# Kernel tuning notes

Measured on AMD Instinct MI355X. Metric: run time of the kernel, lower is better.

The kernel has to match this reference:

```python
import jax, jax.numpy as jnp
import numpy as np
import math

FEAT_DIM = 256
QUERY_DIM = 256
HIDDEN = 64
OUT_DIM = 256
HEADS = 8


def setup_inputs() -> dict:
    key = jax.random.key(0)
    ks = jax.random.split(key, 10)
    B, NQ, NKV = 2, 2048, 2048
    s_q = 1.0 / math.sqrt(QUERY_DIM)
    s_f = 1.0 / math.sqrt(FEAT_DIM)
    s_o = 1.0 / math.sqrt(HIDDEN * HEADS)
    return {
        "feat": jax.random.normal(ks[0], (B, NKV, FEAT_DIM), jnp.float32),
        "query": jax.random.normal(ks[1], (B, NQ, QUERY_DIM), jnp.float32),
        # stacked per-head weights (each head has its own Linear in torch)
        "Wq": jax.random.uniform(ks[2], (HEADS, QUERY_DIM, HIDDEN), jnp.float32, -s_q, s_q),
        "bq": jax.random.uniform(ks[3], (HEADS, HIDDEN), jnp.float32, -s_q, s_q),
        "Wk": jax.random.uniform(ks[4], (HEADS, FEAT_DIM, HIDDEN), jnp.float32, -s_f, s_f),
        "bk": jax.random.uniform(ks[5], (HEADS, HIDDEN), jnp.float32, -s_f, s_f),
        "Wv": jax.random.uniform(ks[6], (HEADS, FEAT_DIM, HIDDEN), jnp.float32, -s_f, s_f),
        "bv": jax.random.uniform(ks[7], (HEADS, HIDDEN), jnp.float32, -s_f, s_f),
        "Wo": jax.random.uniform(ks[8], (HEADS * HIDDEN, OUT_DIM), jnp.float32, -s_o, s_o),
        "bo": jax.random.uniform(ks[9], (OUT_DIM,), jnp.float32, -s_o, s_o),
    }


def reference(feat, query, Wq, bq, Wk, bk, Wv, bv, Wo, bo):
    # Per-head projections, vectorized over the head axis h.
    # q: [B, H, Nq, E]; k, v: [B, H, Nkv, E]
    q = jnp.einsum("bnd,hde->bhne", query, Wq) + bq[None, :, None, :]
    k = jnp.einsum("bnd,hde->bhne", feat, Wk) + bk[None, :, None, :]
    v = jnp.einsum("bnd,hde->bhne", feat, Wv) + bv[None, :, None, :]
    scale = 1.0 / math.sqrt(HIDDEN)
    scores = jnp.einsum("bhqe,bhke->bhqk", q, k) * scale  # [B, H, Nq, Nkv]
    prob = jax.nn.softmax(scores, axis=-1)
    # dropout p=0.0 (eval) -> identity
    heads = jnp.einsum("bhqk,bhke->bhqe", prob, v)  # [B, H, Nq, E]
    # concat heads in order (head 0 first) then output projection
    B, H, NQ, E = heads.shape
    cat = heads.transpose(0, 2, 1, 3).reshape(B, NQ, H * E)
    return cat @ Wo + bo
```

## Files before the change

kernel.cpp:

```cpp
#include <hip/hip_runtime.h>
#include <hip/hip_bf16.h>

typedef unsigned short u16;
typedef __attribute__((ext_vector_type(8))) short short8;
typedef __attribute__((ext_vector_type(4))) float f32x4;
typedef __attribute__((ext_vector_type(16))) float f32x16;
typedef __attribute__((ext_vector_type(2))) int v2i;

#define HEADS 8
#define HID 64
#define QSCALE 0.18033688011112042f

__device__ inline u16 f2bf(float f){
    unsigned u = __float_as_uint(f);
    unsigned r = (u + 0x7fffu + ((u >> 16) & 1u)) >> 16;
    return (u16)r;
}

__device__ inline int cvtpk(float lo, float hi){
    int r;
    asm("v_cvt_pk_bf16_f32 %0, %1, %2" : "=v"(r) : "v"(lo), "v"(hi));
    return r;
}

__device__ inline float exp2fast(float x){
    float r;
    asm("v_exp_f32 %0, %1" : "=v"(r) : "v"(x));
    return r;
}

__device__ inline float xhalf_max(float x){
    v2i r = __builtin_amdgcn_permlane32_swap(__float_as_int(x), __float_as_int(x), false, false);
    return fmaxf(__int_as_float(r.x), __int_as_float(r.y));
}
__device__ inline float xhalf_sum(float x){
    v2i r = __builtin_amdgcn_permlane32_swap(__float_as_int(x), __float_as_int(x), false, false);
    return __int_as_float(r.x) + __int_as_float(r.y);
}

__global__ __launch_bounds__(256) void prep_weights(
    const float* __restrict__ Wq, const float* __restrict__ Wk,
    const float* __restrict__ Wv, const float* __restrict__ Wo,
    u16* __restrict__ WqT, u16* __restrict__ WkT, u16* __restrict__ WvT,
    u16* __restrict__ WoT)
{
    int id = blockIdx.x * 256 + threadIdx.x;
    if (id < 393216) {
        int w = id / 131072;
        int r = id % 131072;
        int c = r >> 8;
        int d = r & 255;
        const float* W = (w == 0) ? Wq : (w == 1 ? Wk : Wv);
        u16* WT = (w == 0) ? WqT : (w == 1 ? WkT : WvT);
        WT[c * 256 + d] = f2bf(W[(c >> 6) * (256 * 64) + d * 64 + (c & 63)]);
    } else {
        int r = id - 393216;
        int o = r >> 9;
        int k = r & 511;
        WoT[o * 512 + k] = f2bf(Wo[k * 256 + o]);
    }
}

__global__ __launch_bounds__(256) void proj_kernel(
    const float* __restrict__ feat, const float* __restrict__ query,
    const u16* __restrict__ WqT, const u16* __restrict__ WkT, const u16* __restrict__ WvT,
    const float* __restrict__ bq, const float* __restrict__ bk, const float* __restrict__ bv,
    u16* __restrict__ Qb, u16* __restrict__ KVf)
{
    int which = blockIdx.z;
    const float* X = (which == 0) ? query : feat;
    const u16* WT = (which == 0) ? WqT : (which == 1 ? WkT : WvT);
    const float* bias = (which == 0) ? bq : (which == 1 ? bk : bv);
    int m0 = blockIdx.x * 64;
    int n0 = blockIdx.y * 64;
    int t = threadIdx.x;
    int lane = t & 63, w = t >> 6;
    int l15 = lane & 15, kof = (lane >> 4) * 8;

    __shared__ __align__(16) u16 lA[64][72];
    __shared__ __align__(16) u16 lB[64][72];

    f32x4 acc[4] = {};
    for (int kt = 0; kt < 256; kt += 64) {
        #pragma unroll
        for (int i = 0; i < 4; i++) {
            int lin = t + i * 256;
            int row = lin >> 4, c4 = (lin & 15) * 4;
            float4 v = *reinterpret_cast<const float4*>(&X[(m0 + row) * 256 + kt + c4]);
            lA[row][c4 + 0] = f2bf(v.x);
            lA[row][c4 + 1] = f2bf(v.y);
            lA[row][c4 + 2] = f2bf(v.z);
            lA[row][c4 + 3] = f2bf(v.w);
        }
        #pragma unroll
        for (int i = 0; i < 2; i++) {
            int lin = t + i * 256;
            int row = lin >> 3, c8 = (lin & 7) * 8;
            *reinterpret_cast<uint4*>(&lB[row][c8]) =
                *reinterpret_cast<const uint4*>(&WT[(n0 + row) * 256 + kt + c8]);
        }
        __syncthreads();
        #pragma unroll
        for (int ks = 0; ks < 2; ks++) {
            short8 a = *reinterpret_cast<const short8*>(&lA[w * 16 + l15][ks * 32 + kof]);
            #pragma unroll
            for (int nt = 0; nt < 4; nt++) {
                short8 b = *reinterpret_cast<const short8*>(&lB[nt * 16 + l15][ks * 32 + kof]);
                acc[nt] = __builtin_amdgcn_mfma_f32_16x16x32_bf16(a, b, acc[nt], 0, 0, 0);
            }
        }
        __syncthreads();
    }
    #pragma unroll
    for (int nt = 0; nt < 4; nt++) {
        #pragma unroll
        for (int i = 0; i < 4; i++) {
            int mrow = m0 + w * 16 + (lane >> 4) * 4 + i;
            int col = n0 + nt * 16 + l15;
            float val = acc[nt][i] + bias[col];
            int b_ = mrow >> 11, n = mrow & 2047;
            int h = col >> 6, e = col & 63;
            int bh = b_ * 8 + h;
            if (which == 0) {
                Qb[(bh * 2048 + n) * 64 + e] = f2bf(val * QSCALE);
            } else {
                int tile = n >> 6, nl = n & 63;
                size_t base = ((size_t)(bh * 32 + tile)) * 8192;
                size_t idx;
                if (which == 1) {
                    int reg  = ((nl >> 5) << 2) | (e >> 4);
                    int ln   = (nl & 31) | (((e >> 3) & 1) << 5);
                    idx = base + reg * 512 + ln * 8 + (e & 7);
                } else {
                    int reg  = ((e >> 5) << 2) | (nl >> 4);
                    int ln   = (e & 31) | (((nl >> 3) & 1) << 5);
                    idx = base + 4096 + reg * 512 + ln * 8 + (nl & 7);
                }
                KVf[idx] = f2bf(val);
            }
        }
    }
}

__global__ __launch_bounds__(512, 2) void attn_kernel(
    const u16* __restrict__ Qb, const u16* __restrict__ KVf, u16* __restrict__ cat)
{
    int lb = blockIdx.x;
    int chunk = lb >> 4;
    int bh = ((lb & 7) << 1) | ((lb >> 3) & 1);
    int b_ = bh >> 3, head = bh & 7;
    int t = threadIdx.x, lane = t & 63, w = t >> 6;
    int l31 = lane & 31, hh = lane >> 5;
    int sp = w >> 1, kvh = w & 1, wi = w >> 1;
    int q0 = chunk * 128 + sp * 32;

    __shared__ __align__(16) u16 smem[34816];
    u16* tiles = smem;
    float* Ol = (float*)smem;
    float* Ml = (float*)(smem + 33792);
    float* Ll = (float*)(smem + 34304);

    const u16* KVfB = KVf + ((size_t)(bh * 32 + kvh * 16)) * 8192;

    short8 qf[4];
    {
        const u16* qp = Qb + (bh * 2048 + q0 + l31) * 64 + hh * 8;
        #pragma unroll
        for (int kc = 0; kc < 4; kc++)
            qf[kc] = *reinterpret_cast<const short8*>(qp + kc * 16);
    }

    f32x16 o0 = {}, o1 = {};
    float mrun = -1e30f, lrun = 0.0f;

#define PACKP(sb, base, out) {                                              \
        int A0 = cvtpk(sb[base+0], sb[base+1]);                             \
        int B0 = cvtpk(sb[base+4], sb[base+5]);                             \
        v2i r0 = __builtin_amdgcn_permlane32_swap(A0, B0, false, false);    \
        int A1 = cvtpk(sb[base+2], sb[base+3]);                             \
        int B1 = cvtpk(sb[base+6], sb[base+7]);                             \
        v2i r1 = __builtin_amdgcn_permlane32_swap(A1, B1, false, false);    \
        union { int i[4]; short8 s; } uu;                                   \
        uu.i[0] = r0.x; uu.i[1] = r1.x; uu.i[2] = r0.y; uu.i[3] = r1.y;     \
        out = uu.s; }

    auto stage = [&](int buf, int tile) {
        const u16* gsrc = KVfB + (size_t)tile * 8192;
        u16* ldst = tiles + (kvh * 2 + buf) * 8192;
        #pragma unroll
        for (int c = 0; c < 4; c++) {
            int off = (wi * 4 + c) * 512 + lane * 8;
            __builtin_amdgcn_global_load_lds(
                (const __attribute__((address_space(1))) unsigned int*)(const void*)(gsrc + off),
                (__attribute__((address_space(3))) unsigned int*)(void*)(ldst + off),
                16, 0, 0);
        }
    };

    stage(0, 0);
    asm volatile("s_waitcnt vmcnt(0)" ::: "memory");
    __syncthreads();

    int cur = 0;
    for (int tt = 0; tt < 16; tt++) {
        if (tt < 15) stage(cur ^ 1, tt + 1);

        const u16* kbase = tiles + (kvh * 2 + cur) * 8192;
        short8 kf[8], vf[8];
        #pragma unroll
        for (int r = 0; r < 8; r++)
            kf[r] = *reinterpret_cast<const short8*>(kbase + r * 512 + lane * 8);
        #pragma unroll
        for (int r = 0; r < 8; r++)
            vf[r] = *reinterpret_cast<const short8*>(kbase + 4096 + r * 512 + lane * 8);

        f32x16 s0 = {}, s1 = {};
        #pragma unroll
        for (int kc = 0; kc < 4; kc++)
            s0 = __builtin_amdgcn_mfma_f32_32x32x16_bf16(kf[kc], qf[kc], s0, 0, 0, 0);
        #pragma unroll
        for (int kc = 0; kc < 4; kc++)
            s1 = __builtin_amdgcn_mfma_f32_32x32x16_bf16(kf[4 + kc], qf[kc], s1, 0, 0, 0);

        float pm[8];
        #pragma unroll
        for (int r = 0; r < 8; r++)
            pm[r] = fmaxf(fmaxf(s0[r], s0[r + 8]), fmaxf(s1[r], s1[r + 8]));
        #pragma unroll
        for (int st = 4; st > 0; st >>= 1)
            #pragma unroll
            for (int r = 0; r < 8; r++) if (r < st) pm[r] = fmaxf(pm[r], pm[r + st]);
        float pmax = xhalf_max(pm[0]);
        if (__any(pmax > mrun + 6.0f)) {
            float mnew = fmaxf(mrun, pmax);
            float corr = exp2fast(mrun - mnew);
            mrun = mnew;
            lrun *= corr;
            #pragma unroll
            for (int r = 0; r < 16; r++) { o0[r] *= corr; o1[r] *= corr; }
        }
        float ac[4] = {0.f, 0.f, 0.f, 0.f};
        #pragma unroll
        for (int r = 0; r < 16; r++) {
            float p0 = exp2fast(s0[r] - mrun);
            float p1 = exp2fast(s1[r] - mrun);
            s0[r] = p0; s1[r] = p1;
            ac[r & 3] += p0 + p1;
        }
        float lsum = (ac[0] + ac[1]) + (ac[2] + ac[3]);
        lrun += xhalf_sum(lsum);

        short8 pf[4];
        PACKP(s0, 0, pf[0]); PACKP(s0, 8, pf[1]);
        PACKP(s1, 0, pf[2]); PACKP(s1, 8, pf[3]);

        #pragma unroll
        for (int c = 0; c < 4; c++) {
            o0 = __builtin_amdgcn_mfma_f32_32x32x16_bf16(vf[c],     pf[c], o0, 0, 0, 0);
            o1 = __builtin_amdgcn_mfma_f32_32x32x16_bf16(vf[4 + c], pf[c], o1, 0, 0, 0);
        }

        asm volatile("s_waitcnt vmcnt(0)" ::: "memory");
        __syncthreads();
        cur ^= 1;
    }

    #pragma unroll
    for (int eb = 0; eb < 2; eb++) {
        #pragma unroll
        for (int r = 0; r < 16; r++) {
            int d = eb * 32 + (r & 3) + 8 * (r >> 2) + 4 * hh;
            Ol[(w * 64 + d) * 33 + l31] = eb ? o1[r] : o0[r];
        }
    }
    if (hh == 0) { Ml[w * 32 + l31] = mrun; Ll[w * 32 + l31] = lrun; }
    __syncthreads();

    {
        int msp = t >> 7;
        int tt2 = t & 127;
        int q = tt2 >> 2;
        int d0 = (tt2 & 3) * 16;
        int wA = msp * 2, wB = msp * 2 + 1;
        float mA = Ml[wA * 32 + q], mB = Ml[wB * 32 + q];
        float ms = fmaxf(mA, mB);
        float scA = exp2fast(mA - ms), scB = exp2fast(mB - ms);
        float lsum = Ll[wA * 32 + q] * scA + Ll[wB * 32 + q] * scB;
        float linv = 1.0f / lsum;
        float vv[16];
        #pragma unroll
        for (int j = 0; j < 16; j++)
            vv[j] = (Ol[(wA * 64 + d0 + j) * 33 + q] * scA +
                     Ol[(wB * 64 + d0 + j) * 33 + q] * scB) * linv;
        uint4 st0, st1;
        st0.x = (unsigned)cvtpk(vv[0],  vv[1]);
        st0.y = (unsigned)cvtpk(vv[2],  vv[3]);
        st0.z = (unsigned)cvtpk(vv[4],  vv[5]);
        st0.w = (unsigned)cvtpk(vv[6],  vv[7]);
        st1.x = (unsigned)cvtpk(vv[8],  vv[9]);
        st1.y = (unsigned)cvtpk(vv[10], vv[11]);
        st1.z = (unsigned)cvtpk(vv[12], vv[13]);
        st1.w = (unsigned)cvtpk(vv[14], vv[15]);
        u16* crow = cat + (b_ * 2048 + chunk * 128 + msp * 32 + q) * 512 + head * 64 + d0;
        *reinterpret_cast<uint4*>(crow) = st0;
        *reinterpret_cast<uint4*>(crow + 8) = st1;
    }
#undef PACKP
}

__global__ __launch_bounds__(256) void outproj_kernel(
    const u16* __restrict__ cat, const u16* __restrict__ WoT,
    const float* __restrict__ bo, float* __restrict__ out)
{
    int m0 = blockIdx.x * 64, n0 = blockIdx.y * 64;
    int t = threadIdx.x, lane = t & 63, w = t >> 6;
    int l15 = lane & 15, kof = (lane >> 4) * 8;

    __shared__ __align__(16) u16 lA[64][72];
    __shared__ __align__(16) u16 lB[64][72];

    f32x4 acc[4] = {};
    for (int kt = 0; kt < 512; kt += 64) {
        #pragma unroll
        for (int i = 0; i < 2; i++) {
            int lin = t + i * 256;
            int row = lin >> 3, c8 = (lin & 7) * 8;
            *reinterpret_cast<uint4*>(&lA[row][c8]) =
                *reinterpret_cast<const uint4*>(&cat[(m0 + row) * 512 + kt + c8]);
            *reinterpret_cast<uint4*>(&lB[row][c8]) =
                *reinterpret_cast<const uint4*>(&WoT[(n0 + row) * 512 + kt + c8]);
        }
        __syncthreads();
        #pragma unroll
        for (int ks = 0; ks < 2; ks++) {
            short8 a = *reinterpret_cast<const short8*>(&lA[w * 16 + l15][ks * 32 + kof]);
            #pragma unroll
            for (int nt = 0; nt < 4; nt++) {
                short8 b = *reinterpret_cast<const short8*>(&lB[nt * 16 + l15][ks * 32 + kof]);
                acc[nt] = __builtin_amdgcn_mfma_f32_16x16x32_bf16(a, b, acc[nt], 0, 0, 0);
            }
        }
        __syncthreads();
    }
    #pragma unroll
    for (int i = 0; i < 4; i++) {
        int mrow = m0 + w * 16 + (lane >> 4) * 4 + i;
        #pragma unroll
        for (int nt = 0; nt < 4; nt++) {
            int col = n0 + nt * 16 + l15;
            out[mrow * 256 + col] = acc[nt][i] + bo[col];
        }
    }
}

extern "C" void kernel_launch(void* const* d_in, const int* in_sizes, int n_in,
                              void* d_out, int out_size, void* d_ws, size_t ws_size,
                              hipStream_t stream) {
    const float* feat  = (const float*)d_in[0];
    const float* query = (const float*)d_in[1];
    const float* Wq = (const float*)d_in[2];
    const float* bq = (const float*)d_in[3];
    const float* Wk = (const float*)d_in[4];
    const float* bk = (const float*)d_in[5];
    const float* Wv = (const float*)d_in[6];
    const float* bv = (const float*)d_in[7];
    const float* Wo = (const float*)d_in[8];
    const float* bo = (const float*)d_in[9];
    float* out = (float*)d_out;

    char* ws = (char*)d_ws;
    u16* WqT = (u16*)(ws + 0);
    u16* WkT = (u16*)(ws + 262144);
    u16* WvT = (u16*)(ws + 524288);
    u16* WoT = (u16*)(ws + 786432);
    u16* Qb  = (u16*)(ws + 1048576);
    u16* KVf = (u16*)(ws + 1048576 + 4194304);
    u16* cat = (u16*)(ws + 1048576 + 12582912);

    hipLaunchKernelGGL(prep_weights, dim3(2048), dim3(256), 0, stream,
                       Wq, Wk, Wv, Wo, WqT, WkT, WvT, WoT);
    hipLaunchKernelGGL(proj_kernel, dim3(64, 8, 3), dim3(256), 0, stream,
                       feat, query, WqT, WkT, WvT, bq, bk, bv, Qb, KVf);
    hipLaunchKernelGGL(attn_kernel, dim3(256), dim3(512), 0, stream,
                       Qb, KVf, cat);
    hipLaunchKernelGGL(outproj_kernel, dim3(64, 4), dim3(256), 0, stream,
                       cat, WoT, bo, out);
}
```

Baseline: 57.62 us.

## Pre-convert activations to bf16 and split attention into smaller 256-thread blocks

Activation fp32->bf16 conversion moves into the prep kernel, so the projection GEMM loads bf16 tiles directly instead of converting them 8-12 times across blocks. The attention kernel is halved to 4 waves and 64 queries per block, doubling the grid to 512 blocks for better CU coverage, at the cost of reloading K/V tiles more often. MFMA sections are also wrapped with s_setprio to favour matrix issue. This adds an extra global round trip for the bf16 activations.

```diff
diff --git a/kernel.cpp b/kernel.cpp
--- a/kernel.cpp
+++ b/kernel.cpp
@@ -39,22 +39,37 @@
 }
 
 __global__ __launch_bounds__(256) void prep_weights(
+    const float* __restrict__ query, const float* __restrict__ feat,
     const float* __restrict__ Wq, const float* __restrict__ Wk,
     const float* __restrict__ Wv, const float* __restrict__ Wo,
+    u16* __restrict__ Xbq, u16* __restrict__ Xbf,
     u16* __restrict__ WqT, u16* __restrict__ WkT, u16* __restrict__ WvT,
     u16* __restrict__ WoT)
 {
     int id = blockIdx.x * 256 + threadIdx.x;
-    if (id < 393216) {
-        int w = id / 131072;
-        int r = id % 131072;
+    if (id < 262144) {
+        const float* src = (id < 131072) ? query : feat;
+        u16* dst = (id < 131072) ? Xbq : Xbf;
+        int r = (id < 131072) ? id : id - 131072;
+        float4 a = *reinterpret_cast<const float4*>(&src[r * 8]);
+        float4 b = *reinterpret_cast<const float4*>(&src[r * 8 + 4]);
+        uint4 s;
+        s.x = (unsigned)cvtpk(a.x, a.y);
+        s.y = (unsigned)cvtpk(a.z, a.w);
+        s.z = (unsigned)cvtpk(b.x, b.y);
+        s.w = (unsigned)cvtpk(b.z, b.w);
+        *reinterpret_cast<uint4*>(&dst[r * 8]) = s;
+    } else if (id < 655360) {
+        int id2 = id - 262144;
+        int w = id2 / 131072;
+        int r = id2 % 131072;
         int c = r >> 8;
         int d = r & 255;
         const float* W = (w == 0) ? Wq : (w == 1 ? Wk : Wv);
         u16* WT = (w == 0) ? WqT : (w == 1 ? WkT : WvT);
         WT[c * 256 + d] = f2bf(W[(c >> 6) * (256 * 64) + d * 64 + (c & 63)]);
     } else {
-        int r = id - 393216;
+        int r = id - 655360;
         int o = r >> 9;
         int k = r & 511;
         WoT[o * 512 + k] = f2bf(Wo[k * 256 + o]);
@@ -62,13 +77,13 @@
 }
 
 __global__ __launch_bounds__(256) void proj_kernel(
-    const float* __restrict__ feat, const float* __restrict__ query,
+    const u16* __restrict__ Xbq, const u16* __restrict__ Xbf,
     const u16* __restrict__ WqT, const u16* __restrict__ WkT, const u16* __restrict__ WvT,
     const float* __restrict__ bq, const float* __restrict__ bk, const float* __restrict__ bv,
     u16* __restrict__ Qb, u16* __restrict__ KVf)
 {
     int which = blockIdx.z;
-    const float* X = (which == 0) ? query : feat;
+    const u16* Xb = (which == 0) ? Xbq : Xbf;
     const u16* WT = (which == 0) ? WqT : (which == 1 ? WkT : WvT);
     const float* bias = (which == 0) ? bq : (which == 1 ? bk : bv);
     int m0 = blockIdx.x * 64;
@@ -83,19 +98,11 @@
     f32x4 acc[4] = {};
     for (int kt = 0; kt < 256; kt += 64) {
         #pragma unroll
-        for (int i = 0; i < 4; i++) {
-            int lin = t + i * 256;
-            int row = lin >> 4, c4 = (lin & 15) * 4;
-            float4 v = *reinterpret_cast<const float4*>(&X[(m0 + row) * 256 + kt + c4]);
-            lA[row][c4 + 0] = f2bf(v.x);
-            lA[row][c4 + 1] = f2bf(v.y);
-            lA[row][c4 + 2] = f2bf(v.z);
-            lA[row][c4 + 3] = f2bf(v.w);
-        }
-        #pragma unroll
         for (int i = 0; i < 2; i++) {
             int lin = t + i * 256;
             int row = lin >> 3, c8 = (lin & 7) * 8;
+            *reinterpret_cast<uint4*>(&lA[row][c8]) =
+                *reinterpret_cast<const uint4*>(&Xb[(m0 + row) * 256 + kt + c8]);
             *reinterpret_cast<uint4*>(&lB[row][c8]) =
                 *reinterpret_cast<const uint4*>(&WT[(n0 + row) * 256 + kt + c8]);
         }
@@ -142,7 +149,7 @@
     }
 }
 
-__global__ __launch_bounds__(512, 2) void attn_kernel(
+__global__ __launch_bounds__(256, 2) void attn_kernel(
     const u16* __restrict__ Qb, const u16* __restrict__ KVf, u16* __restrict__ cat)
 {
     int lb = blockIdx.x;
@@ -151,14 +158,14 @@
     int b_ = bh >> 3, head = bh & 7;
     int t = threadIdx.x, lane = t & 63, w = t >> 6;
     int l31 = lane & 31, hh = lane >> 5;
-    int sp = w >> 1, kvh = w & 1, wi = w >> 1;
-    int q0 = chunk * 128 + sp * 32;
-
-    __shared__ __align__(16) u16 smem[34816];
+    int sp = w >> 1, kvh = w & 1;
+    int q0 = chunk * 64 + sp * 32;
+
+    __shared__ __align__(16) u16 smem[32768];
     u16* tiles = smem;
     float* Ol = (float*)smem;
-    float* Ml = (float*)(smem + 33792);
-    float* Ll = (float*)(smem + 34304);
+    float* Ml = (float*)(smem + 16896);
+    float* Ll = (float*)(smem + 17152);
 
     const u16* KVfB = KVf + ((size_t)(bh * 32 + kvh * 16)) * 8192;
 
@@ -188,8 +195,8 @@
         const u16* gsrc = KVfB + (size_t)tile * 8192;
         u16* ldst = tiles + (kvh * 2 + buf) * 8192;
         #pragma unroll
-        for (int c = 0; c < 4; c++) {
-            int off = (wi * 4 + c) * 512 + lane * 8;
+        for (int c = 0; c < 8; c++) {
+            int off = (sp * 8 + c) * 512 + lane * 8;
             __builtin_amdgcn_global_load_lds(
                 (const __attribute__((address_space(1))) unsigned int*)(const void*)(gsrc + off),
                 (__attribute__((address_space(3))) unsigned int*)(void*)(ldst + off),
@@ -215,12 +222,14 @@
             vf[r] = *reinterpret_cast<const short8*>(kbase + 4096 + r * 512 + lane * 8);
 
         f32x16 s0 = {}, s1 = {};
+        __builtin_amdgcn_s_setprio(1);
         #pragma unroll
         for (int kc = 0; kc < 4; kc++)
             s0 = __builtin_amdgcn_mfma_f32_32x32x16_bf16(kf[kc], qf[kc], s0, 0, 0, 0);
         #pragma unroll
         for (int kc = 0; kc < 4; kc++)
             s1 = __builtin_amdgcn_mfma_f32_32x32x16_bf16(kf[4 + kc], qf[kc], s1, 0, 0, 0);
+        __builtin_amdgcn_s_setprio(0);
 
         float pm[8];
         #pragma unroll
@@ -254,11 +263,13 @@
         PACKP(s0, 0, pf[0]); PACKP(s0, 8, pf[1]);
         PACKP(s1, 0, pf[2]); PACKP(s1, 8, pf[3]);
 
+        __builtin_amdgcn_s_setprio(1);
         #pragma unroll
         for (int c = 0; c < 4; c++) {
             o0 = __builtin_amdgcn_mfma_f32_32x32x16_bf16(vf[c],     pf[c], o0, 0, 0, 0);
             o1 = __builtin_amdgcn_mfma_f32_32x32x16_bf16(vf[4 + c], pf[c], o1, 0, 0, 0);
         }
+        __builtin_amdgcn_s_setprio(0);
 
         asm volatile("s_waitcnt vmcnt(0)" ::: "memory");
         __syncthreads();
@@ -301,7 +312,7 @@
         st1.y = (unsigned)cvtpk(vv[10], vv[11]);
         st1.z = (unsigned)cvtpk(vv[12], vv[13]);
         st1.w = (unsigned)cvtpk(vv[14], vv[15]);
-        u16* crow = cat + (b_ * 2048 + chunk * 128 + msp * 32 + q) * 512 + head * 64 + d0;
+        u16* crow = cat + (b_ * 2048 + chunk * 64 + msp * 32 + q) * 512 + head * 64 + d0;
         *reinterpret_cast<uint4*>(crow) = st0;
         *reinterpret_cast<uint4*>(crow + 8) = st1;
     }
@@ -374,14 +385,16 @@
     u16* WvT = (u16*)(ws + 524288);
     u16* WoT = (u16*)(ws + 786432);
     u16* Qb  = (u16*)(ws + 1048576);
-    u16* KVf = (u16*)(ws + 1048576 + 4194304);
-    u16* cat = (u16*)(ws + 1048576 + 12582912);
-
-    hipLaunchKernelGGL(prep_weights, dim3(2048), dim3(256), 0, stream,
-                       Wq, Wk, Wv, Wo, WqT, WkT, WvT, WoT);
+    u16* KVf = (u16*)(ws + 5242880);
+    u16* cat = (u16*)(ws + 13631488);
+    u16* Xbq = (u16*)(ws + 17825792);
+    u16* Xbf = (u16*)(ws + 19922944);
+
+    hipLaunchKernelGGL(prep_weights, dim3(3072), dim3(256), 0, stream,
+                       query, feat, Wq, Wk, Wv, Wo, Xbq, Xbf, WqT, WkT, WvT, WoT);
     hipLaunchKernelGGL(proj_kernel, dim3(64, 8, 3), dim3(256), 0, stream,
-                       feat, query, WqT, WkT, WvT, bq, bk, bv, Qb, KVf);
-    hipLaunchKernelGGL(attn_kernel, dim3(256), dim3(512), 0, stream,
+                       Xbq, Xbf, WqT, WkT, WvT, bq, bk, bv, Qb, KVf);
+    hipLaunchKernelGGL(attn_kernel, dim3(512), dim3(256), 0, stream,
                        Qb, KVf, cat);
     hipLaunchKernelGGL(outproj_kernel, dim3(64, 4), dim3(256), 0, stream,
                        cat, WoT, bo, out);
```

Result: slower. 59.36 us (+3.0%).
